# Kernel tuning notes

Measured on AMD Instinct MI355X. Metric: run time of the kernel, lower is better.

The kernel has to match this reference:

```python
import jax, jax.numpy as jnp
import numpy as np

B, T, S1, S2 = 4, 256, 256, 256
D = 512          # tgt_dims == src_dims
V = 32000        # tgt_voc_size
H, DH = 8, 64    # heads, head_dims; HID = H*DH == D
HID = H * DH
VEXT = V + S1 + S2


def layer_norm(x):
    m = jnp.mean(x, axis=-1, keepdims=True)
    v = jnp.mean((x - m) ** 2, axis=-1, keepdims=True)
    return (x - m) / jnp.sqrt(v + 1e-5)


def copy_attention(query, key, qmask, kmask, Wq, bq, Wk, bk, Wv, bv, Wo, bo):
    # conv1d with kernel 1 == linear; weights are [out, in]
    b, t, _ = query.shape
    s = key.shape[1]
    q = (query @ Wq.T + bq).reshape(b, t, H, DH).transpose(0, 2, 1, 3) * (DH ** -0.5)
    k = (key @ Wk.T + bk).reshape(b, s, H, DH).transpose(0, 2, 1, 3)
    v = (key @ Wv.T + bv).reshape(b, s, H, DH).transpose(0, 2, 1, 3)
    att = jnp.einsum('bhtd,bhkd->bhtk', q, k)            # [B,H,T,S]
    out_att = att * kmask[:, None, None, :]              # multiplicative mask copy
    att = jnp.where((kmask == 0)[:, None, None, :], -jnp.inf, att)
    att = jax.nn.softmax(att, axis=-1)
    out = jnp.einsum('bhtk,bhkd->bhtd', att, v)
    out = out.transpose(0, 2, 1, 3).reshape(b, t, HID)
    out = (out @ Wo.T + bo) * qmask[:, :, None]
    out_att = out_att * qmask[:, None, :, None]
    return out_att.mean(axis=1), out                     # [B,T,S], [B,T,D]


def scatter_copy(att, map_idx):
    # copy_output[b, t, map_idx[b, s]] += att[b, t, s]  (accumulate=True)
    b, t, s = att.shape
    bi = jnp.arange(b)[:, None, None]
    ti = jnp.arange(t)[None, :, None]
    out = jnp.zeros((b, t, VEXT), att.dtype)
    return out.at[bi, ti, map_idx[:, None, :]].add(att)


def setup_inputs() -> dict:
    key = jax.random.key(0)
    ks = jax.random.split(key, 24)
    p = 0.02
    inp = {
        'tgt_dec_out': jax.random.normal(ks[0], (B, T, D), jnp.float32),
        'src1_key': jax.random.normal(ks[1], (B, S1, D), jnp.float32),
        'src1_map_idx': jax.random.randint(ks[2], (B, S1), 0, VEXT),
        'src2_key': jax.random.normal(ks[3], (B, S2, D), jnp.float32),
        'src2_map_idx': jax.random.randint(ks[4], (B, S2), 0, VEXT),
        'Wfc': jax.random.normal(ks[5], (V, D), jnp.float32) * p,
        'bfc': jnp.zeros((V,), jnp.float32),
        'Wp': jax.random.normal(ks[6], (3, 3 * D), jnp.float32) * p,
        'bp': jnp.zeros((3,), jnp.float32),
    }
    i = 7
    for a in ('1', '2'):
        for nm in ('Wq', 'Wk', 'Wv', 'Wo'):
            inp[nm + a] = jax.random.normal(ks[i], (HID, D), jnp.float32) * p
            inp[nm.replace('W', 'b') + a] = jnp.zeros((HID,), jnp.float32)
            i += 1
    return inp


def reference(tgt_dec_out, src1_key, src1_map_idx, src2_key, src2_map_idx,
              Wfc, bfc, Wp, bp,
              Wq1, bq1, Wk1, bk1, Wv1, bv1, Wo1, bo1,
              Wq2, bq2, Wk2, bk2, Wv2, bv2, Wo2, bo2):
    tgt_output = layer_norm(tgt_dec_out @ Wfc.T + bfc)          # [B,T,V]
    tgt_output = jnp.pad(tgt_output, ((0, 0), (0, 0), (0, S1 + S2)))  # [B,T,VEXT]
    tgt_mask = jnp.sign(jnp.abs(tgt_dec_out).sum(-1))
    src1_mask = jnp.sign(jnp.abs(src1_key).sum(-1))
    src2_mask = jnp.sign(jnp.abs(src2_key).sum(-1))
    att1, c1 = copy_attention(tgt_dec_out, src1_key, tgt_mask, src1_mask,
                              Wq1, bq1, Wk1, bk1, Wv1, bv1, Wo1, bo1)
    copy1 = scatter_copy(layer_norm(att1), src1_map_idx)
    att2, c2 = copy_attention(tgt_dec_out, src2_key, tgt_mask, src2_mask,
                              Wq2, bq2, Wk2, bk2, Wv2, bv2, Wo2, bo2)
    copy2 = scatter_copy(layer_norm(att2), src2_map_idx)
    p = jax.nn.softmax(jnp.concatenate([tgt_dec_out, c1, c2], axis=-1) @ Wp.T + bp, axis=-1)  # [B,T,3]
    out = tgt_output * p[..., 0:1] + copy1 * p[..., 1:2] + copy2 * p[..., 2:3]
    return out
```

## Files before the change

kernel.cpp:

```cpp
#include <hip/hip_runtime.h>
#include <hip/hip_bf16.h>
#include <cstdint>
#include <cstddef>

#define B_     4
#define T_     256
#define S_     256
#define D_     512
#define V_     32000
#define H_     8
#define DH_    64
#define HID_   512
#define VEXT_  32512
#define BT_    1024
#define CHUNK_ 8192
#define NSEG_  23

typedef __hip_bfloat16 bf16;
typedef __bf16 bf16x8 __attribute__((ext_vector_type(8)));
typedef float  f32x4  __attribute__((ext_vector_type(4)));

__device__ inline void store_val(float* p, float v) { *p = v; }
__device__ inline void store_val(bf16* p, float v)  { *p = __float2bfloat16(v); }

__device__ inline float bfbits2f(unsigned short u) {
    return __uint_as_float(((unsigned)u) << 16);
}
__device__ inline unsigned short f2bfbits(float f) {
    bf16 h = __float2bfloat16(f);
    union { bf16 h; unsigned short u; } cv; cv.h = h; return cv.u;
}

__global__ void probe_kernel(const unsigned short* __restrict__ x, int* __restrict__ flag,
                             float* __restrict__ rsum, float* __restrict__ rsq)
{
    __shared__ int cnt;
    if (threadIdx.x == 0) cnt = 0;
    __syncthreads();
    for (int i = threadIdx.x; i < BT_; i += 256) { rsum[i] = 0.f; rsq[i] = 0.f; }
    int c = 0;
    for (int i = threadIdx.x; i < 4096; i += 256) {
        const int e = (x[i] >> 7) & 0xFF;
        if (e >= 96 && e <= 159) c++;
    }
    atomicAdd(&cnt, c);
    __syncthreads();
    if (threadIdx.x == 0) *flag = (cnt < 3500) ? 1 : 0;
}

struct ConvArgs {
    const void* src[NSEG_];
    void*       dst[NSEG_];
};

__global__ __launch_bounds__(256)
void convert_all_kernel(ConvArgs a, const int* __restrict__ flag)
{
    const int CNT[NSEG_] = {
        524288, 524288, 524288, 32000, 4608, 3,
        262144, 262144, 512, 512,
        262144, 262144, 512, 512,
        262144, 262144, 512, 512,
        262144, 512, 262144, 512,
        16384000
    };
    const int fm = *flag;
    int seg = 0, blk = blockIdx.x;
    for (;;) {
        const int nb = (CNT[seg] + 8191) >> 13;
        if (blk < nb) break;
        blk -= nb; seg++;
    }
    const int n    = CNT[seg];
    const int j0   = blk << 13;
    const int jend = (n < j0 + 8192) ? n : (j0 + 8192);
    if (fm) {
        const float* s = (const float*)a.src[seg];
        unsigned short* d = (unsigned short*)a.dst[seg];
        for (int j = j0 + threadIdx.x * 4; j < jend; j += 1024) {
            if (j + 4 <= jend) {
                float4 v = *(const float4*)(s + j);
                ushort4 u;
                u.x = f2bfbits(v.x); u.y = f2bfbits(v.y);
                u.z = f2bfbits(v.z); u.w = f2bfbits(v.w);
                *(ushort4*)(d + j) = u;
            } else {
                for (int t = j; t < jend; t++) d[t] = f2bfbits(s[t]);
            }
        }
    } else {
        const unsigned short* s = (const unsigned short*)a.src[seg];
        unsigned short* d = (unsigned short*)a.dst[seg];
        for (int j = j0 + threadIdx.x * 4; j < jend; j += 1024) {
            if (j + 4 <= jend) {
                *(ushort4*)(d + j) = *(const ushort4*)(s + j);
            } else {
                for (int t = j; t < jend; t++) d[t] = s[t];
            }
        }
    }
}

__global__ void masks_kernel(const bf16* __restrict__ tgt, const bf16* __restrict__ s1,
                             const bf16* __restrict__ s2, float* __restrict__ mt,
                             float* __restrict__ m1, float* __restrict__ m2)
{
    const int row = blockIdx.x;
    const bf16* src; float* dst;
    if (row < BT_)           { src = tgt + (size_t)row * D_;            dst = mt + row; }
    else if (row < 2 * BT_)  { src = s1 + (size_t)(row - BT_) * D_;     dst = m1 + (row - BT_); }
    else                     { src = s2 + (size_t)(row - 2 * BT_) * D_; dst = m2 + (row - 2 * BT_); }
    const int lane = threadIdx.x;
    float s = 0.f;
    for (int i = lane; i < D_; i += 64) s += fabsf(__bfloat162float(src[i]));
#pragma unroll
    for (int off = 32; off; off >>= 1) s += __shfl_down(s, off);
    if (lane == 0) *dst = (s > 0.f) ? 1.f : 0.f;
}

template <typename OutT>
__device__ __forceinline__
void gemm_tile_body(const bf16* __restrict__ A, const bf16* __restrict__ Bw,
                    const bf16* __restrict__ bias, OutT* __restrict__ C,
                    const int K, const int ldC, const int m0, const int n0,
                    bf16* As, bf16* Bs)
{
    const int tid  = threadIdx.x;
    const int lane = tid & 63;
    const int wave = tid >> 6;
    const int quad = lane >> 4, l16 = lane & 15;
    const int wm = (wave >> 1) * 64, wn = (wave & 1) * 64;

    f32x4 acc[4][4];
#pragma unroll
    for (int i = 0; i < 4; i++)
#pragma unroll
        for (int j = 0; j < 4; j++) acc[i][j] = (f32x4){0.f, 0.f, 0.f, 0.f};

    const int row0 = tid >> 2;
    const int kp   = (tid & 3) * 8;
    const int sw   = (row0 & 3) << 3;
    const int swf  = (l16 & 3) << 3;

    for (int k0 = 0; k0 < K; k0 += 32) {
        uint4 a0 = *(const uint4*)(A  + (size_t)(m0 + row0)      * K + k0 + kp);
        uint4 a1 = *(const uint4*)(A  + (size_t)(m0 + row0 + 64) * K + k0 + kp);
        uint4 b0 = *(const uint4*)(Bw + (size_t)(n0 + row0)      * K + k0 + kp);
        uint4 b1 = *(const uint4*)(Bw + (size_t)(n0 + row0 + 64) * K + k0 + kp);
        __syncthreads();
        *(uint4*)(As + row0 * 32 + (kp ^ sw))        = a0;
        *(uint4*)(As + (row0 + 64) * 32 + (kp ^ sw)) = a1;
        *(uint4*)(Bs + row0 * 32 + (kp ^ sw))        = b0;
        *(uint4*)(Bs + (row0 + 64) * 32 + (kp ^ sw)) = b1;
        __syncthreads();

        bf16x8 af[4], bfv[4];
#pragma unroll
        for (int i = 0; i < 4; i++)
            af[i] = *(const bf16x8*)(As + (wm + i * 16 + l16) * 32 + ((quad * 8) ^ swf));
#pragma unroll
        for (int j = 0; j < 4; j++)
            bfv[j] = *(const bf16x8*)(Bs + (wn + j * 16 + l16) * 32 + ((quad * 8) ^ swf));
#pragma unroll
        for (int i = 0; i < 4; i++)
#pragma unroll
            for (int j = 0; j < 4; j++)
                acc[i][j] = __builtin_amdgcn_mfma_f32_16x16x32_bf16(af[i], bfv[j], acc[i][j], 0, 0, 0);
    }

#pragma unroll
    for (int i = 0; i < 4; i++)
#pragma unroll
        for (int j = 0; j < 4; j++) {
            const int nb = n0 + wn + j * 16 + l16;
            const float bv = __bfloat162float(bias[nb]);
#pragma unroll
            for (int r = 0; r < 4; r++) {
                const int m = m0 + wm + i * 16 + quad * 4 + r;
                store_val(C + (size_t)m * ldC + nb, acc[i][j][r] + bv);
            }
        }
}

struct Proj3Args {
    const bf16* A[3];
    const bf16* W[3];
    const bf16* b[3];
    bf16*       C[3];
};

__global__ __launch_bounds__(256)
void gemm_proj3_kernel(Proj3Args pa)
{
    __shared__ bf16 As[128 * 32];
    __shared__ bf16 Bs[128 * 32];
    const int z = blockIdx.z;
    gemm_tile_body<bf16>(pa.A[z], pa.W[z], pa.b[z], pa.C[z], D_, 1024,
                         blockIdx.y * 128, blockIdx.x * 128, As, Bs);
}

struct Out2Args {
    const bf16* A[2];
    const bf16* W[2];
    const bf16* b[2];
    float*      C[2];
};

__global__ __launch_bounds__(256)
void gemm_out2_kernel(Out2Args oa)
{
    __shared__ bf16 As[128 * 32];
    __shared__ bf16 Bs[128 * 32];
    const int z = blockIdx.z;
    gemm_tile_body<float>(oa.A[z], oa.W[z], oa.b[z], oa.C[z], D_, HID_,
                          blockIdx.y * 128, blockIdx.x * 128, As, Bs);
}

__global__ __launch_bounds__(256)
void gemm_fc_kernel(const bf16* __restrict__ A, const bf16* __restrict__ Bw,
                    const bf16* __restrict__ bias, void* __restrict__ Cv,
                    const int* __restrict__ flag,
                    float* __restrict__ rsum, float* __restrict__ rsq)
{
    __shared__ bf16 As[128 * 32];
    __shared__ bf16 Bs[128 * 32];
    const int fm = *flag;
    const int tid  = threadIdx.x;
    const int lane = tid & 63;
    const int wave = tid >> 6;
    const int quad = lane >> 4, l16 = lane & 15;
    const int f  = (blockIdx.x & 7) * 250 + (blockIdx.x >> 3);
    const int m0 = (f & 7) * 128;
    const int n0 = (f >> 3) * 128;
    const int wm = (wave >> 1) * 64, wn = (wave & 1) * 64;

    f32x4 acc[4][4];
#pragma unroll
    for (int i = 0; i < 4; i++)
#pragma unroll
        for (int j = 0; j < 4; j++) acc[i][j] = (f32x4){0.f, 0.f, 0.f, 0.f};

    const int row0 = tid >> 2;
    const int kp   = (tid & 3) * 8;
    const int sw   = (row0 & 3) << 3;
    const int swf  = (l16 & 3) << 3;

    for (int k0 = 0; k0 < D_; k0 += 32) {
        uint4 a0 = *(const uint4*)(A  + (size_t)(m0 + row0)      * D_ + k0 + kp);
        uint4 a1 = *(const uint4*)(A  + (size_t)(m0 + row0 + 64) * D_ + k0 + kp);
        uint4 b0 = *(const uint4*)(Bw + (size_t)(n0 + row0)      * D_ + k0 + kp);
        uint4 b1 = *(const uint4*)(Bw + (size_t)(n0 + row0 + 64) * D_ + k0 + kp);
        __syncthreads();
        *(uint4*)(As + row0 * 32 + (kp ^ sw))        = a0;
        *(uint4*)(As + (row0 + 64) * 32 + (kp ^ sw)) = a1;
        *(uint4*)(Bs + row0 * 32 + (kp ^ sw))        = b0;
        *(uint4*)(Bs + (row0 + 64) * 32 + (kp ^ sw)) = b1;
        __syncthreads();

        bf16x8 af[4], bfv[4];
#pragma unroll
        for (int i = 0; i < 4; i++)
            af[i] = *(const bf16x8*)(As + (wm + i * 16 + l16) * 32 + ((quad * 8) ^ swf));
#pragma unroll
        for (int j = 0; j < 4; j++)
            bfv[j] = *(const bf16x8*)(Bs + (wn + j * 16 + l16) * 32 + ((quad * 8) ^ swf));
#pragma unroll
        for (int i = 0; i < 4; i++)
#pragma unroll
            for (int j = 0; j < 4; j++)
                acc[i][j] = __builtin_amdgcn_mfma_f32_16x16x32_bf16(af[i], bfv[j], acc[i][j], 0, 0, 0);
    }

    float srow[4][4], sqr[4][4];
#pragma unroll
    for (int i = 0; i < 4; i++)
#pragma unroll
        for (int r = 0; r < 4; r++) { srow[i][r] = 0.f; sqr[i][r] = 0.f; }

#pragma unroll
    for (int i = 0; i < 4; i++)
#pragma unroll
        for (int j = 0; j < 4; j++) {
            const int nb = n0 + wn + j * 16 + l16;
            const float bv = __bfloat162float(bias[nb]);
#pragma unroll
            for (int r = 0; r < 4; r++) {
                const int m = m0 + wm + i * 16 + quad * 4 + r;
                const float val = acc[i][j][r] + bv;
                if (fm) ((float*)Cv)[(size_t)m * VEXT_ + nb] = val;
                else    ((bf16*)Cv)[(size_t)m * VEXT_ + nb] = __float2bfloat16(val);
                srow[i][r] += val;
                sqr[i][r]  += val * val;
            }
        }

#pragma unroll
    for (int i = 0; i < 4; i++)
#pragma unroll
        for (int r = 0; r < 4; r++) {
            float s = srow[i][r], q = sqr[i][r];
#pragma unroll
            for (int off = 1; off <= 8; off <<= 1) {
                s += __shfl_xor(s, off);
                q += __shfl_xor(q, off);
            }
            if (l16 == 0) {
                const int m = m0 + wm + i * 16 + quad * 4 + r;
                atomicAdd(&rsum[m], s);
                atomicAdd(&rsq[m],  q);
            }
        }
}

__global__ __launch_bounds__(256)
void fused_attn2_kernel(const bf16* __restrict__ qcat,
                        const bf16* __restrict__ kv1, const bf16* __restrict__ kv2,
                        const float* __restrict__ qmask,
                        const float* __restrict__ km1, const float* __restrict__ km2,
                        bf16* __restrict__ ctx1, bf16* __restrict__ ctx2,
                        float* __restrict__ lno1, float* __restrict__ lno2)
{
    __shared__ float qs[4][HID_];
    __shared__ float pvs[4][H_][260];
    const int y = blockIdx.y;
    const bf16* qb = qcat + y * HID_;
    const bf16* kv = y ? kv2 : kv1;
    const float* kmask = y ? km2 : km1;
    bf16* ctx = y ? ctx2 : ctx1;
    float* lnout = y ? lno2 : lno1;

    const int tid = threadIdx.x;
    const int lane = tid & 63, wv = tid >> 6;
    const int bt = blockIdx.x * 4 + wv;
    const int b  = bt >> 8;

    {
        const bf16* qp = qb + (size_t)bt * 1024 + lane * 8;
        ushort4 u0 = *(const ushort4*)(qp);
        ushort4 u1 = *(const ushort4*)(qp + 4);
        float* qd = &qs[wv][lane * 8];
        qd[0] = bfbits2f(u0.x) * 0.125f; qd[1] = bfbits2f(u0.y) * 0.125f;
        qd[2] = bfbits2f(u0.z) * 0.125f; qd[3] = bfbits2f(u0.w) * 0.125f;
        qd[4] = bfbits2f(u1.x) * 0.125f; qd[5] = bfbits2f(u1.y) * 0.125f;
        qd[6] = bfbits2f(u1.z) * 0.125f; qd[7] = bfbits2f(u1.w) * 0.125f;
    }

    float kmv[4]; bool on[4];
#pragma unroll
    for (int i = 0; i < 4; i++) {
        kmv[i] = kmask[b * S_ + lane + 64 * i];
        on[i] = kmv[i] != 0.f;
    }

    const bf16* kbase = kv + (size_t)(b * S_ + lane) * 1024;
    float msum[4] = {0.f, 0.f, 0.f, 0.f};

    for (int h = 0; h < H_; h++) {
        const float* qh = &qs[wv][h * DH_];
        float sc[4] = {0.f, 0.f, 0.f, 0.f};
#pragma unroll
        for (int d0 = 0; d0 < DH_; d0 += 8) {
            const float qv0 = qh[d0 + 0], qv1 = qh[d0 + 1], qv2 = qh[d0 + 2], qv3 = qh[d0 + 3];
            const float qv4 = qh[d0 + 4], qv5 = qh[d0 + 5], qv6 = qh[d0 + 6], qv7 = qh[d0 + 7];
#pragma unroll
            for (int i = 0; i < 4; i++) {
                const bf16* kp = kbase + (size_t)i * 64 * 1024 + h * DH_ + d0;
                ushort4 u0 = *(const ushort4*)(kp);
                ushort4 u1 = *(const ushort4*)(kp + 4);
                sc[i] += qv0 * bfbits2f(u0.x) + qv1 * bfbits2f(u0.y)
                       + qv2 * bfbits2f(u0.z) + qv3 * bfbits2f(u0.w)
                       + qv4 * bfbits2f(u1.x) + qv5 * bfbits2f(u1.y)
                       + qv6 * bfbits2f(u1.z) + qv7 * bfbits2f(u1.w);
            }
        }
        float xs[4];
        float mx = -INFINITY;
#pragma unroll
        for (int i = 0; i < 4; i++) {
            msum[i] += sc[i];
            xs[i] = on[i] ? sc[i] : -INFINITY;
            mx = fmaxf(mx, xs[i]);
        }
#pragma unroll
        for (int off = 32; off; off >>= 1) mx = fmaxf(mx, __shfl_xor(mx, off));
        float e[4], ts = 0.f;
        const bool live = (mx > -INFINITY);
#pragma unroll
        for (int i = 0; i < 4; i++) {
            e[i] = (on[i] && live) ? __expf(xs[i] - mx) : 0.f;
            ts += e[i];
        }
#pragma unroll
        for (int off = 32; off; off >>= 1) ts += __shfl_xor(ts, off);
        const float inv = (ts > 0.f) ? 1.f / ts : 0.f;
#pragma unroll
        for (int i = 0; i < 4; i++)
            pvs[wv][h][lane + 64 * i] = e[i] * inv;
    }

    {
        const float* prow = pvs[wv][lane >> 3];
        const bf16* vp = kv + (size_t)(b * S_) * 1024 + 512 + lane * 8;
        float o0 = 0.f, o1 = 0.f, o2 = 0.f, o3 = 0.f, o4 = 0.f, o5 = 0.f, o6 = 0.f, o7 = 0.f;
#pragma unroll 8
        for (int s = 0; s < S_; s++) {
            ushort4 u0 = *(const ushort4*)(vp + (size_t)s * 1024);
            ushort4 u1 = *(const ushort4*)(vp + (size_t)s * 1024 + 4);
            const float pv = prow[s];
            o0 += pv * bfbits2f(u0.x); o1 += pv * bfbits2f(u0.y);
            o2 += pv * bfbits2f(u0.z); o3 += pv * bfbits2f(u0.w);
            o4 += pv * bfbits2f(u1.x); o5 += pv * bfbits2f(u1.y);
            o6 += pv * bfbits2f(u1.z); o7 += pv * bfbits2f(u1.w);
        }
        ushort4 w0, w1;
        w0.x = f2bfbits(o0); w0.y = f2bfbits(o1); w0.z = f2bfbits(o2); w0.w = f2bfbits(o3);
        w1.x = f2bfbits(o4); w1.y = f2bfbits(o5); w1.z = f2bfbits(o6); w1.w = f2bfbits(o7);
        bf16* cp = ctx + (size_t)bt * HID_ + lane * 8;
        *(ushort4*)(cp) = w0;
        *(ushort4*)(cp + 4) = w1;
    }

    const float qm = qmask[bt];
    float am[4], s1 = 0.f;
#pragma unroll
    for (int i = 0; i < 4; i++) {
        am[i] = msum[i] * (1.f / H_) * kmv[i] * qm;
        s1 += am[i];
    }
#pragma unroll
    for (int off = 32; off; off >>= 1) s1 += __shfl_xor(s1, off);
    const float mean = s1 * (1.f / S_);
    float dv = 0.f;
#pragma unroll
    for (int i = 0; i < 4; i++) dv += (am[i] - mean) * (am[i] - mean);
#pragma unroll
    for (int off = 32; off; off >>= 1) dv += __shfl_xor(dv, off);
    const float rstd = rsqrtf(fmaxf(dv * (1.f / S_), 0.f) + 1e-5f);
#pragma unroll
    for (int i = 0; i < 4; i++)
        lnout[(size_t)bt * S_ + lane + 64 * i] = (am[i] - mean) * rstd;
}

__global__ void pgate_kernel(const bf16* __restrict__ x, const float* __restrict__ c1,
                             const float* __restrict__ c2, const float* __restrict__ qmask,
                             const bf16* __restrict__ Wp, const bf16* __restrict__ bp,
                             float* __restrict__ p)
{
    const int bt = blockIdx.x;
    const int lane = threadIdx.x;
    const float qm = qmask[bt];
    float a0 = 0.f, a1 = 0.f, a2 = 0.f;
    for (int d = lane; d < D_; d += 64) {
        const float xv  = __bfloat162float(x[(size_t)bt * D_ + d]);
        const float c1v = c1[(size_t)bt * D_ + d] * qm;
        const float c2v = c2[(size_t)bt * D_ + d] * qm;
        a0 += xv * __bfloat162float(Wp[0 * 3 * D_ + d])
            + c1v * __bfloat162float(Wp[0 * 3 * D_ + D_ + d])
            + c2v * __bfloat162float(Wp[0 * 3 * D_ + 2 * D_ + d]);
        a1 += xv * __bfloat162float(Wp[1 * 3 * D_ + d])
            + c1v * __bfloat162float(Wp[1 * 3 * D_ + D_ + d])
            + c2v * __bfloat162float(Wp[1 * 3 * D_ + 2 * D_ + d]);
        a2 += xv * __bfloat162float(Wp[2 * 3 * D_ + d])
            + c1v * __bfloat162float(Wp[2 * 3 * D_ + D_ + d])
            + c2v * __bfloat162float(Wp[2 * 3 * D_ + 2 * D_ + d]);
    }
#pragma unroll
    for (int off = 32; off; off >>= 1) {
        a0 += __shfl_down(a0, off);
        a1 += __shfl_down(a1, off);
        a2 += __shfl_down(a2, off);
    }
    if (lane == 0) {
        float l0 = a0 + __bfloat162float(bp[0]);
        float l1 = a1 + __bfloat162float(bp[1]);
        float l2 = a2 + __bfloat162float(bp[2]);
        float mx = fmaxf(l0, fmaxf(l1, l2));
        float e0 = __expf(l0 - mx), e1 = __expf(l1 - mx), e2 = __expf(l2 - mx);
        float inv = 1.f / (e0 + e1 + e2);
        p[bt * 3 + 0] = e0 * inv; p[bt * 3 + 1] = e1 * inv; p[bt * 3 + 2] = e2 * inv;
    }
}

__global__ __launch_bounds__(256)
void final_kernel(void* __restrict__ outv, const int* __restrict__ flag,
                  const float* __restrict__ ln1, const float* __restrict__ ln2,
                  const int* __restrict__ map1, const int* __restrict__ map2,
                  const float* __restrict__ p,
                  const float* __restrict__ rsum, const float* __restrict__ rsq)
{
    __shared__ float chnk[CHUNK_];
    const int fm = *flag;
    const int bt = blockIdx.x, b = bt >> 8, tid = threadIdx.x;
    const float p0 = p[bt * 3], p1 = p[bt * 3 + 1], p2 = p[bt * 3 + 2];
    const float m = rsum[bt] * (1.f / V_);
    const float var = fmaxf(rsq[bt] * (1.f / V_) - m * m, 0.f);
    const float r = rsqrtf(var + 1e-5f);
    const size_t rbase = (size_t)bt * VEXT_;

    for (int c = 0; c < 4; c++) {
        const int jlo = c * CHUNK_;
        const int n = (VEXT_ - jlo < CHUNK_) ? (VEXT_ - jlo) : CHUNK_;
        for (int jj = tid * 4; jj < n; jj += 1024) {
            const int j = jlo + jj;
            float4 fv = {0.f, 0.f, 0.f, 0.f};
            if (j < V_) {
                float v0, v1, v2, v3;
                if (fm) {
                    float4 u = *(const float4*)((const float*)outv + rbase + j);
                    v0 = u.x; v1 = u.y; v2 = u.z; v3 = u.w;
                } else {
                    ushort4 u = *(const ushort4*)((const unsigned short*)outv + rbase + j);
                    v0 = bfbits2f(u.x); v1 = bfbits2f(u.y); v2 = bfbits2f(u.z); v3 = bfbits2f(u.w);
                }
                fv.x = p0 * (v0 - m) * r;
                fv.y = p0 * (v1 - m) * r;
                fv.z = p0 * (v2 - m) * r;
                fv.w = p0 * (v3 - m) * r;
            }
            *(float4*)(chnk + jj) = fv;
        }
        __syncthreads();
        for (int e = tid; e < 2 * S_; e += 256) {
            const int src = e >> 8, si = e & 255;
            const int j = (src ? map2 : map1)[b * S_ + si];
            if (j >= jlo && j < jlo + n) {
                const float val = (src ? p2 : p1) * (src ? ln2 : ln1)[(size_t)bt * S_ + si];
                atomicAdd(&chnk[j - jlo], val);
            }
        }
        __syncthreads();
        if (fm) {
            float* orow = (float*)outv + rbase;
            for (int jj = tid * 4; jj < n; jj += 1024)
                *(float4*)(orow + jlo + jj) = *(const float4*)(chnk + jj);
        } else {
            unsigned short* orow = (unsigned short*)outv + rbase;
            for (int jj = tid * 4; jj < n; jj += 1024) {
                float4 v = *(const float4*)(chnk + jj);
                ushort4 u;
                u.x = f2bfbits(v.x); u.y = f2bfbits(v.y); u.z = f2bfbits(v.z); u.w = f2bfbits(v.w);
                *(ushort4*)(orow + jlo + jj) = u;
            }
        }
        __syncthreads();
    }
}

extern "C" void kernel_launch(void* const* d_in, const int* in_sizes, int n_in,
                              void* d_out, int out_size, void* d_ws, size_t ws_size,
                              hipStream_t stream)
{
    const int* map1 = (const int*)d_in[2];
    const int* map2 = (const int*)d_in[4];

    char* w = (char*)d_ws;
    size_t off = 0;
    auto carve = [&](size_t bytes) -> char* {
        char* ptr = w + off;
        off = (off + bytes + 255) & ~(size_t)255;
        return ptr;
    };
    int* flag = (int*)carve(16);

    bf16* xc   = (bf16*)carve((size_t)BT_ * D_ * 2);
    bf16* s1c  = (bf16*)carve((size_t)B_ * S_ * D_ * 2);
    bf16* s2c  = (bf16*)carve((size_t)B_ * S_ * D_ * 2);
    bf16* Wfcc = (bf16*)carve((size_t)V_ * D_ * 2);
    bf16* bfcc = (bf16*)carve((size_t)V_ * 2);
    bf16* Wpc  = (bf16*)carve((size_t)3 * 3 * D_ * 2);
    bf16* bpc  = (bf16*)carve(3 * 2);
    bf16* Wqq  = (bf16*)carve((size_t)2 * HID_ * D_ * 2);
    bf16* bqq  = (bf16*)carve((size_t)2 * HID_ * 2);
    bf16* Wkv1 = (bf16*)carve((size_t)2 * HID_ * D_ * 2);
    bf16* bkv1 = (bf16*)carve((size_t)2 * HID_ * 2);
    bf16* Wkv2 = (bf16*)carve((size_t)2 * HID_ * D_ * 2);
    bf16* bkv2 = (bf16*)carve((size_t)2 * HID_ * 2);
    bf16* Wo1c = (bf16*)carve((size_t)HID_ * D_ * 2);
    bf16* bo1c = (bf16*)carve((size_t)HID_ * 2);
    bf16* Wo2c = (bf16*)carve((size_t)HID_ * D_ * 2);
    bf16* bo2c = (bf16*)carve((size_t)HID_ * 2);

    bf16*  qcat = (bf16*) carve((size_t)BT_ * 1024 * 2);
    bf16*  kv1  = (bf16*) carve((size_t)BT_ * 1024 * 2);
    bf16*  kv2  = (bf16*) carve((size_t)BT_ * 1024 * 2);
    bf16*  ctx1 = (bf16*) carve((size_t)BT_ * HID_ * 2);
    bf16*  ctx2 = (bf16*) carve((size_t)BT_ * HID_ * 2);
    float* c1   = (float*)carve((size_t)BT_ * HID_ * 4);
    float* c2   = (float*)carve((size_t)BT_ * HID_ * 4);
    float* ln1  = (float*)carve((size_t)BT_ * S_ * 4);
    float* ln2  = (float*)carve((size_t)BT_ * S_ * 4);
    float* p    = (float*)carve((size_t)BT_ * 3 * 4);
    float* mt   = (float*)carve((size_t)BT_ * 4);
    float* m1   = (float*)carve((size_t)BT_ * 4);
    float* m2   = (float*)carve((size_t)BT_ * 4);
    float* rsum = (float*)carve((size_t)BT_ * 4);
    float* rsq  = (float*)carve((size_t)BT_ * 4);
    (void)ws_size; (void)in_sizes; (void)n_in; (void)out_size;

    probe_kernel<<<1, 256, 0, stream>>>((const unsigned short*)d_in[0], flag, rsum, rsq);

    ConvArgs ca;
    ca.src[0]  = d_in[0];  ca.dst[0]  = xc;
    ca.src[1]  = d_in[1];  ca.dst[1]  = s1c;
    ca.src[2]  = d_in[3];  ca.dst[2]  = s2c;
    ca.src[3]  = d_in[6];  ca.dst[3]  = bfcc;
    ca.src[4]  = d_in[7];  ca.dst[4]  = Wpc;
    ca.src[5]  = d_in[8];  ca.dst[5]  = bpc;
    ca.src[6]  = d_in[9];  ca.dst[6]  = Wqq;
    ca.src[7]  = d_in[17]; ca.dst[7]  = Wqq + (size_t)HID_ * D_;
    ca.src[8]  = d_in[10]; ca.dst[8]  = bqq;
    ca.src[9]  = d_in[18]; ca.dst[9]  = bqq + HID_;
    ca.src[10] = d_in[11]; ca.dst[10] = Wkv1;
    ca.src[11] = d_in[13]; ca.dst[11] = Wkv1 + (size_t)HID_ * D_;
    ca.src[12] = d_in[12]; ca.dst[12] = bkv1;
    ca.src[13] = d_in[14]; ca.dst[13] = bkv1 + HID_;
    ca.src[14] = d_in[19]; ca.dst[14] = Wkv2;
    ca.src[15] = d_in[21]; ca.dst[15] = Wkv2 + (size_t)HID_ * D_;
    ca.src[16] = d_in[20]; ca.dst[16] = bkv2;
    ca.src[17] = d_in[22]; ca.dst[17] = bkv2 + HID_;
    ca.src[18] = d_in[15]; ca.dst[18] = Wo1c;
    ca.src[19] = d_in[16]; ca.dst[19] = bo1c;
    ca.src[20] = d_in[23]; ca.dst[20] = Wo2c;
    ca.src[21] = d_in[24]; ca.dst[21] = bo2c;
    ca.src[22] = d_in[5];  ca.dst[22] = Wfcc;
    convert_all_kernel<<<2462, 256, 0, stream>>>(ca, flag);

    masks_kernel<<<3 * BT_, 64, 0, stream>>>(xc, s1c, s2c, mt, m1, m2);

    gemm_fc_kernel<<<2000, 256, 0, stream>>>(xc, Wfcc, bfcc, d_out, flag, rsum, rsq);

    Proj3Args pa;
    pa.A[0] = xc;   pa.W[0] = Wqq;  pa.b[0] = bqq;  pa.C[0] = qcat;
    pa.A[1] = s1c;  pa.W[1] = Wkv1; pa.b[1] = bkv1; pa.C[1] = kv1;
    pa.A[2] = s2c;  pa.W[2] = Wkv2; pa.b[2] = bkv2; pa.C[2] = kv2;
    gemm_proj3_kernel<<<dim3(1024 / 128, BT_ / 128, 3), 256, 0, stream>>>(pa);

    fused_attn2_kernel<<<dim3(BT_ / 4, 2), 256, 0, stream>>>(qcat, kv1, kv2, mt, m1, m2,
                                                             ctx1, ctx2, ln1, ln2);

    Out2Args oa;
    oa.A[0] = ctx1; oa.W[0] = Wo1c; oa.b[0] = bo1c; oa.C[0] = c1;
    oa.A[1] = ctx2; oa.W[1] = Wo2c; oa.b[1] = bo2c; oa.C[1] = c2;
    gemm_out2_kernel<<<dim3(HID_ / 128, BT_ / 128, 2), 256, 0, stream>>>(oa);

    pgate_kernel<<<BT_, 64, 0, stream>>>(xc, c1, c2, mt, Wpc, bpc, p);

    final_kernel<<<BT_, 256, 0, stream>>>(d_out, flag, ln1, ln2, map1, map2, p, rsum, rsq);
}
```

Baseline: 496.9 us.

## Split attention QK^T into separate MFMA GEMM kernel writing scores buffer

The fused attention kernel computed Q·K scores with scalar FP32 dot products that read K from global memory per wave. This moves the QK^T product into a dedicated batched MFMA bf16 GEMM kernel that writes scaled fp32 scores to a 16 MB workspace buffer, and the softmax/PV kernel then reads those scores. The aim is to replace scalar ALU work with matrix cores, at the cost of an extra launch and a round trip of the score tensor through memory.

```diff
diff --git a/kernel.cpp b/kernel.cpp
--- a/kernel.cpp
+++ b/kernel.cpp
@@ -313,17 +313,85 @@
 }
 
 __global__ __launch_bounds__(256)
-void fused_attn2_kernel(const bf16* __restrict__ qcat,
-                        const bf16* __restrict__ kv1, const bf16* __restrict__ kv2,
-                        const float* __restrict__ qmask,
-                        const float* __restrict__ km1, const float* __restrict__ km2,
-                        bf16* __restrict__ ctx1, bf16* __restrict__ ctx2,
-                        float* __restrict__ lno1, float* __restrict__ lno2)
-{
-    __shared__ float qs[4][HID_];
+void attn_qk_kernel(const bf16* __restrict__ qcat, const bf16* __restrict__ kv1,
+                    const bf16* __restrict__ kv2, float* __restrict__ scores)
+{
+    __shared__ bf16 As[128 * 32];
+    __shared__ bf16 Bs[128 * 32];
+    const int tid  = threadIdx.x;
+    const int lane = tid & 63;
+    const int wave = tid >> 6;
+    const int quad = lane >> 4, l16 = lane & 15;
+    const int z = blockIdx.z;
+    const int stream = z >> 5, b = (z >> 3) & 3, h = z & 7;
+    const bf16* kv = stream ? kv2 : kv1;
+    const int m0 = blockIdx.y * 128, n0 = blockIdx.x * 128;
+    const int wm = (wave >> 1) * 64, wn = (wave & 1) * 64;
+
+    f32x4 acc[4][4];
+#pragma unroll
+    for (int i = 0; i < 4; i++)
+#pragma unroll
+        for (int j = 0; j < 4; j++) acc[i][j] = (f32x4){0.f, 0.f, 0.f, 0.f};
+
+    const int row0 = tid >> 2;
+    const int kp   = (tid & 3) * 8;
+    const int sw   = (row0 & 3) << 3;
+    const int swf  = (l16 & 3) << 3;
+
+    const bf16* Abase = qcat + (size_t)(b * 256) * 1024 + stream * 512 + h * 64;
+    const bf16* Bbase = kv   + (size_t)(b * 256) * 1024 + h * 64;
+
+    for (int k0 = 0; k0 < 64; k0 += 32) {
+        uint4 a0 = *(const uint4*)(Abase + (size_t)(m0 + row0)      * 1024 + k0 + kp);
+        uint4 a1 = *(const uint4*)(Abase + (size_t)(m0 + row0 + 64) * 1024 + k0 + kp);
+        uint4 b0 = *(const uint4*)(Bbase + (size_t)(n0 + row0)      * 1024 + k0 + kp);
+        uint4 b1 = *(const uint4*)(Bbase + (size_t)(n0 + row0 + 64) * 1024 + k0 + kp);
+        __syncthreads();
+        *(uint4*)(As + row0 * 32 + (kp ^ sw))        = a0;
+        *(uint4*)(As + (row0 + 64) * 32 + (kp ^ sw)) = a1;
+        *(uint4*)(Bs + row0 * 32 + (kp ^ sw))        = b0;
+        *(uint4*)(Bs + (row0 + 64) * 32 + (kp ^ sw)) = b1;
+        __syncthreads();
+
+        bf16x8 af[4], bfv[4];
+#pragma unroll
+        for (int i = 0; i < 4; i++)
+            af[i] = *(const bf16x8*)(As + (wm + i * 16 + l16) * 32 + ((quad * 8) ^ swf));
+#pragma unroll
+        for (int j = 0; j < 4; j++)
+            bfv[j] = *(const bf16x8*)(Bs + (wn + j * 16 + l16) * 32 + ((quad * 8) ^ swf));
+#pragma unroll
+        for (int i = 0; i < 4; i++)
+#pragma unroll
+            for (int j = 0; j < 4; j++)
+                acc[i][j] = __builtin_amdgcn_mfma_f32_16x16x32_bf16(af[i], bfv[j], acc[i][j], 0, 0, 0);
+    }
+
+    float* sp = scores + (size_t)z * 65536;
+#pragma unroll
+    for (int i = 0; i < 4; i++)
+#pragma unroll
+        for (int j = 0; j < 4; j++) {
+            const int nb = n0 + wn + j * 16 + l16;
+#pragma unroll
+            for (int r = 0; r < 4; r++) {
+                const int m = m0 + wm + i * 16 + quad * 4 + r;
+                sp[(size_t)m * 256 + nb] = acc[i][j][r] * 0.125f;
+            }
+        }
+}
+
+__global__ __launch_bounds__(256)
+void attn_sm_kernel(const float* __restrict__ scores,
+                    const bf16* __restrict__ kv1, const bf16* __restrict__ kv2,
+                    const float* __restrict__ qmask,
+                    const float* __restrict__ km1, const float* __restrict__ km2,
+                    bf16* __restrict__ ctx1, bf16* __restrict__ ctx2,
+                    float* __restrict__ lno1, float* __restrict__ lno2)
+{
     __shared__ float pvs[4][H_][260];
     const int y = blockIdx.y;
-    const bf16* qb = qcat + y * HID_;
     const bf16* kv = y ? kv2 : kv1;
     const float* kmask = y ? km2 : km1;
     bf16* ctx = y ? ctx2 : ctx1;
@@ -332,18 +400,7 @@
     const int tid = threadIdx.x;
     const int lane = tid & 63, wv = tid >> 6;
     const int bt = blockIdx.x * 4 + wv;
-    const int b  = bt >> 8;
-
-    {
-        const bf16* qp = qb + (size_t)bt * 1024 + lane * 8;
-        ushort4 u0 = *(const ushort4*)(qp);
-        ushort4 u1 = *(const ushort4*)(qp + 4);
-        float* qd = &qs[wv][lane * 8];
-        qd[0] = bfbits2f(u0.x) * 0.125f; qd[1] = bfbits2f(u0.y) * 0.125f;
-        qd[2] = bfbits2f(u0.z) * 0.125f; qd[3] = bfbits2f(u0.w) * 0.125f;
-        qd[4] = bfbits2f(u1.x) * 0.125f; qd[5] = bfbits2f(u1.y) * 0.125f;
-        qd[6] = bfbits2f(u1.z) * 0.125f; qd[7] = bfbits2f(u1.w) * 0.125f;
-    }
+    const int b  = bt >> 8, t = bt & 255;
 
     float kmv[4]; bool on[4];
 #pragma unroll
@@ -352,27 +409,15 @@
         on[i] = kmv[i] != 0.f;
     }
 
-    const bf16* kbase = kv + (size_t)(b * S_ + lane) * 1024;
+    const float* sbase = scores + (size_t)(y * 32 + b * 8) * 65536 + (size_t)t * 256;
     float msum[4] = {0.f, 0.f, 0.f, 0.f};
 
     for (int h = 0; h < H_; h++) {
-        const float* qh = &qs[wv][h * DH_];
-        float sc[4] = {0.f, 0.f, 0.f, 0.f};
-#pragma unroll
-        for (int d0 = 0; d0 < DH_; d0 += 8) {
-            const float qv0 = qh[d0 + 0], qv1 = qh[d0 + 1], qv2 = qh[d0 + 2], qv3 = qh[d0 + 3];
-            const float qv4 = qh[d0 + 4], qv5 = qh[d0 + 5], qv6 = qh[d0 + 6], qv7 = qh[d0 + 7];
-#pragma unroll
-            for (int i = 0; i < 4; i++) {
-                const bf16* kp = kbase + (size_t)i * 64 * 1024 + h * DH_ + d0;
-                ushort4 u0 = *(const ushort4*)(kp);
-                ushort4 u1 = *(const ushort4*)(kp + 4);
-                sc[i] += qv0 * bfbits2f(u0.x) + qv1 * bfbits2f(u0.y)
-                       + qv2 * bfbits2f(u0.z) + qv3 * bfbits2f(u0.w)
-                       + qv4 * bfbits2f(u1.x) + qv5 * bfbits2f(u1.y)
-                       + qv6 * bfbits2f(u1.z) + qv7 * bfbits2f(u1.w);
-            }
-        }
+        const float* sp = sbase + (size_t)h * 65536;
+        float sc[4];
+#pragma unroll
+        for (int i = 0; i < 4; i++) sc[i] = sp[lane + 64 * i];
+
         float xs[4];
         float mx = -INFINITY;
 #pragma unroll
@@ -595,6 +640,7 @@
     float* m2   = (float*)carve((size_t)BT_ * 4);
     float* rsum = (float*)carve((size_t)BT_ * 4);
     float* rsq  = (float*)carve((size_t)BT_ * 4);
+    float* scr  = (float*)carve((size_t)64 * 65536 * 4);
     (void)ws_size; (void)in_sizes; (void)n_in; (void)out_size;
 
     probe_kernel<<<1, 256, 0, stream>>>((const unsigned short*)d_in[0], flag, rsum, rsq);
@@ -635,8 +681,10 @@
     pa.A[2] = s2c;  pa.W[2] = Wkv2; pa.b[2] = bkv2; pa.C[2] = kv2;
     gemm_proj3_kernel<<<dim3(1024 / 128, BT_ / 128, 3), 256, 0, stream>>>(pa);
 
-    fused_attn2_kernel<<<dim3(BT_ / 4, 2), 256, 0, stream>>>(qcat, kv1, kv2, mt, m1, m2,
-                                                             ctx1, ctx2, ln1, ln2);
+    attn_qk_kernel<<<dim3(2, 2, 64), 256, 0, stream>>>(qcat, kv1, kv2, scr);
+
+    attn_sm_kernel<<<dim3(BT_ / 4, 2), 256, 0, stream>>>(scr, kv1, kv2, mt, m1, m2,
+                                                         ctx1, ctx2, ln1, ln2);
 
     Out2Args oa;
     oa.A[0] = ctx1; oa.W[0] = Wo1c; oa.b[0] = bo1c; oa.C[0] = c1;
```

Result: faster. 432.6 us (-12.9%).
